# Kernel optimization log

Hardware: AMD Instinct MI355X
Metric: run time of the kernel (lower is better)

## Reference

```python
import jax, jax.numpy as jnp
import numpy as np
from functools import partial

V, CTX, D, H, L, FF = 50257, 1024, 768, 12, 12, 3072
DH = D // H
EPS = 1e-5


def _ln(x, g, b):
    m = jnp.mean(x, axis=-1, keepdims=True)
    v = jnp.mean(jnp.square(x - m), axis=-1, keepdims=True)
    return (x - m) * jax.lax.rsqrt(v + EPS) * g + b


def setup_inputs() -> dict:
    key = jax.random.key(0)
    ks = jax.random.split(key, 8)
    s = 0.02
    return {
        "input_ids": jax.random.randint(ks[0], (2, 1024), 0, V),
        "token_emb": jax.random.normal(ks[1], (V, D), jnp.float32) * s,
        "pos_emb": jax.random.normal(ks[2], (CTX, D), jnp.float32) * s,
        "ln1_g": jnp.ones((L, D), jnp.float32),
        "ln1_b": jnp.zeros((L, D), jnp.float32),
        "qkv_w": jax.random.normal(ks[3], (L, 3 * D, D), jnp.float32) * s,
        "out_w": jax.random.normal(ks[4], (L, D, D), jnp.float32) * (s / np.sqrt(2 * L)),
        "ln2_g": jnp.ones((L, D), jnp.float32),
        "ln2_b": jnp.zeros((L, D), jnp.float32),
        "ff1_w": jax.random.normal(ks[5], (L, FF, D), jnp.float32) * s,
        "ff2_w": jax.random.normal(ks[6], (L, D, FF), jnp.float32) * s,
        "lnf_g": jnp.ones((D,), jnp.float32),
        "lnf_b": jnp.zeros((D,), jnp.float32),
    }


def reference(input_ids, token_emb, pos_emb, ln1_g, ln1_b, qkv_w, out_w,
              ln2_g, ln2_b, ff1_w, ff2_w, lnf_g, lnf_b):
    B, T = input_ids.shape
    x = token_emb[input_ids] + pos_emb[:T]  # [B,T,D]
    causal = jnp.tril(jnp.ones((T, T), bool))  # True = keep
    scale = 1.0 / np.sqrt(DH)

    def block(x, p):
        g1, b1, wqkv, wo, g2, b2, w1, w2 = p
        h = _ln(x, g1, b1)
        qkv = h @ wqkv.T  # [B,T,3D]
        q, k, v = jnp.split(qkv, 3, axis=-1)
        q = q.reshape(B, T, H, DH).transpose(0, 2, 1, 3)
        k = k.reshape(B, T, H, DH).transpose(0, 2, 1, 3)
        v = v.reshape(B, T, H, DH).transpose(0, 2, 1, 3)
        scores = jnp.einsum('bhqd,bhkd->bhqk', q, k) * scale
        scores = jnp.where(causal, scores, -jnp.inf)
        w = jax.nn.softmax(scores, axis=-1)
        o = jnp.einsum('bhqk,bhkd->bhqd', w, v)
        o = o.transpose(0, 2, 1, 3).reshape(B, T, D) @ wo.T
        x = x + o
        h2 = _ln(x, g2, b2)
        ff = jax.nn.gelu(h2 @ w1.T, approximate=False) @ w2.T
        return x + ff, None

    params = (ln1_g, ln1_b, qkv_w, out_w, ln2_g, ln2_b, ff1_w, ff2_w)
    x, _ = jax.lax.scan(block, x, params)
    x = _ln(x, lnf_g, lnf_b)
    logits = x @ token_emb.T  # tied lm head
    return logits
```

## Files before the change

kernel.cpp:

```cpp
#include <hip/hip_runtime.h>
#include <hip/hip_bf16.h>
#include <math.h>

#define D_MODEL 768
#define NHEAD 12
#define DHEAD 64
#define NLAYER 12
#define FF_DIM 3072
#define SEQ 1024
#define TOKENS 2048
#define VOCAB 50257

typedef short bf16x8 __attribute__((ext_vector_type(8)));
typedef float f32x4 __attribute__((ext_vector_type(4)));
typedef unsigned short u16x4 __attribute__((ext_vector_type(4)));
typedef unsigned short u16x8 __attribute__((ext_vector_type(8)));

__device__ inline unsigned short f2bf(float f) {
    union { float f; unsigned u; } un;
    un.f = f;
    unsigned u = un.u;
    u += 0x7fffu + ((u >> 16) & 1u);
    return (unsigned short)(u >> 16);
}

__device__ inline void gl_lds16(const void* g, void* l) {
    __builtin_amdgcn_global_load_lds(
        (const __attribute__((address_space(1))) unsigned int*)g,
        (__attribute__((address_space(3))) unsigned int*)l, 16, 0, 0);
}

__global__ __launch_bounds__(256) void cvt_kernel(const float* __restrict__ s,
                                                  unsigned short* __restrict__ d,
                                                  long n4) {
    long i = (long)blockIdx.x * 256 + threadIdx.x;
    long stride = (long)gridDim.x * 256;
    for (; i < n4; i += stride) {
        f32x4 v = ((const f32x4*)s)[i];
        u16x4 r;
        r[0] = f2bf(v[0]); r[1] = f2bf(v[1]); r[2] = f2bf(v[2]); r[3] = f2bf(v[3]);
        ((u16x4*)d)[i] = r;
    }
}

__global__ __launch_bounds__(256) void embed_kernel(const int* __restrict__ ids,
                                                    const float* __restrict__ tok,
                                                    const float* __restrict__ pos,
                                                    float* __restrict__ x) {
    int i = blockIdx.x * 256 + threadIdx.x;
    int row = i / D_MODEL;
    int d = i - row * D_MODEL;
    int t = row & (SEQ - 1);
    x[i] = tok[(long)ids[row] * D_MODEL + d] + pos[(long)t * D_MODEL + d];
}

__global__ __launch_bounds__(256) void ln_kernel(const float* __restrict__ x,
                                                 const float* __restrict__ g,
                                                 const float* __restrict__ b,
                                                 unsigned short* __restrict__ out) {
    int row = blockIdx.x;
    int tid = threadIdx.x;
    const float* xr = x + (long)row * D_MODEL;
    float v0 = xr[tid], v1 = xr[tid + 256], v2 = xr[tid + 512];
    __shared__ float sm[4];
    float s = v0 + v1 + v2;
    #pragma unroll
    for (int off = 32; off; off >>= 1) s += __shfl_xor(s, off);
    if ((tid & 63) == 0) sm[tid >> 6] = s;
    __syncthreads();
    float mean = (sm[0] + sm[1] + sm[2] + sm[3]) * (1.f / D_MODEL);
    __syncthreads();
    float d0 = v0 - mean, d1 = v1 - mean, d2 = v2 - mean;
    s = d0 * d0 + d1 * d1 + d2 * d2;
    #pragma unroll
    for (int off = 32; off; off >>= 1) s += __shfl_xor(s, off);
    if ((tid & 63) == 0) sm[tid >> 6] = s;
    __syncthreads();
    float var = (sm[0] + sm[1] + sm[2] + sm[3]) * (1.f / D_MODEL);
    float rs = rsqrtf(var + 1e-5f);
    unsigned short* orow = out + (long)row * D_MODEL;
    orow[tid]       = f2bf(d0 * rs * g[tid]       + b[tid]);
    orow[tid + 256] = f2bf(d1 * rs * g[tid + 256] + b[tid + 256]);
    orow[tid + 512] = f2bf(d2 * rs * g[tid + 512] + b[tid + 512]);
}

#define GM_NONE 0
#define GM_RES  1
#define GM_GELU 2
#define GM_QKV  3

template<int WM, int WN, int MODE, bool SWZ>
__global__ __launch_bounds__(256) void gemm_bf16(
        const unsigned short* __restrict__ A, const unsigned short* __restrict__ W,
        int M, int N, int K,
        float* __restrict__ Cf, unsigned short* __restrict__ Cb,
        const float* __restrict__ RES,
        unsigned short* __restrict__ P1, unsigned short* __restrict__ P2) {
    constexpr int BM = WM * 32, BN = WN * 32;
    __shared__ unsigned short lA[BM * 64];
    __shared__ unsigned short lB[BN * 64];

    int tid = threadIdx.x;
    int lane = tid & 63, wv = tid >> 6;
    int wr = wv >> 1, wc = wv & 1;
    int lr = lane & 15, kq = lane >> 4;

    int mtile, ntile;
    if (SWZ) {
        int lb = blockIdx.y * gridDim.x + blockIdx.x;
        int g = lb >> 3, r8 = lb & 7;
        mtile = g % gridDim.x;
        ntile = (g / gridDim.x) * 8 + r8;
        if (ntile * BN >= N) return;
    } else {
        mtile = blockIdx.x;
        ntile = blockIdx.y;
    }
    int row0 = mtile * BM;
    int col0 = ntile * BN;

    int srow_in = tid >> 3;
    int ssp = tid & 7;
    int skg = ssp ^ (srow_in & 7);
    int lbase = ((tid & ~63)) << 3;

    f32x4 acc[WM][WN];
    #pragma unroll
    for (int m = 0; m < WM; m++)
        #pragma unroll
        for (int n = 0; n < WN; n++) acc[m][n] = (f32x4){0.f, 0.f, 0.f, 0.f};

    for (int kt = 0; kt < K; kt += 64) {
        #pragma unroll
        for (int i = 0; i < BM / 32; i++) {
            int row = i * 32 + srow_in;
            gl_lds16(A + (size_t)(row0 + row) * K + kt + skg * 8,
                     &lA[i * 2048 + lbase]);
        }
        #pragma unroll
        for (int i = 0; i < BN / 32; i++) {
            int row = i * 32 + srow_in;
            int srow = col0 + row;
            if (srow >= N) srow = N - 1;
            gl_lds16(W + (size_t)srow * K + kt + skg * 8,
                     &lB[i * 2048 + lbase]);
        }
        __syncthreads();
        #pragma unroll
        for (int kk = 0; kk < 2; kk++) {
            int kg = kk * 4 + kq;
            bf16x8 af[WM], bfr[WN];
            #pragma unroll
            for (int m = 0; m < WM; m++) {
                int row = wr * (WM * 16) + m * 16 + lr;
                af[m] = *(const bf16x8*)&lA[row * 64 + ((kg ^ (row & 7)) << 3)];
            }
            #pragma unroll
            for (int n = 0; n < WN; n++) {
                int row = wc * (WN * 16) + n * 16 + lr;
                bfr[n] = *(const bf16x8*)&lB[row * 64 + ((kg ^ (row & 7)) << 3)];
            }
            #pragma unroll
            for (int m = 0; m < WM; m++)
                #pragma unroll
                for (int n = 0; n < WN; n++)
                    acc[m][n] = __builtin_amdgcn_mfma_f32_16x16x32_bf16(af[m], bfr[n], acc[m][n], 0, 0, 0);
        }
        __syncthreads();
    }

    #pragma unroll
    for (int m = 0; m < WM; m++) {
        int r0 = row0 + wr * (WM * 16) + m * 16 + (kq << 2);
        #pragma unroll
        for (int n = 0; n < WN; n++) {
            int c = col0 + wc * (WN * 16) + n * 16 + lr;
            if (c < N) {
                #pragma unroll
                for (int j = 0; j < 4; j++) {
                    int r = r0 + j;
                    size_t idx = (size_t)r * N + c;
                    float v = acc[m][n][j];
                    if (MODE == GM_RES) {
                        Cf[idx] = v + RES[idx];
                    } else if (MODE == GM_GELU) {
                        Cb[idx] = f2bf(0.5f * v * (1.f + erff(v * 0.70710678118f)));
                    } else if (MODE == GM_QKV) {
                        int bb = r >> 10, t = r & 1023;
                        if (c < D_MODEL) {
                            int h = c >> 6, dh = c & 63;
                            P1[(((size_t)(bb * NHEAD + h) * SEQ) + t) * 64 + dh] = f2bf(v * 0.125f);
                        } else if (c < 2 * D_MODEL) {
                            int cc = c - D_MODEL;
                            int h = cc >> 6, dh = cc & 63;
                            P2[(((size_t)(bb * NHEAD + h) * SEQ) + t) * 64 + dh] = f2bf(v);
                        } else {
                            Cb[(size_t)r * D_MODEL + (c - 2 * D_MODEL)] = f2bf(v);
                        }
                    } else {
                        Cf[idx] = v;
                    }
                }
            }
        }
    }
}

__global__ __launch_bounds__(256) void vprep_kernel(const unsigned short* __restrict__ Vrow,
                                                    unsigned short* __restrict__ Vt) {
    __shared__ unsigned short T[64][66];
    int b = blockIdx.z, h = blockIdx.y, t0 = blockIdx.x * 64;
    int tid = threadIdx.x;
    int tin = tid >> 2, seg = tid & 3;
    const unsigned short* src = Vrow + ((size_t)(b * SEQ) + t0 + tin) * D_MODEL
                                + h * 64 + seg * 16;
    u16x8 a0 = *(const u16x8*)src;
    u16x8 a1 = *(const u16x8*)(src + 8);
    #pragma unroll
    for (int e = 0; e < 8; e++) { T[tin][seg * 16 + e] = a0[e]; T[tin][seg * 16 + 8 + e] = a1[e]; }
    __syncthreads();
    int dh = tid >> 2;
    unsigned short* dst = Vt + ((size_t)(b * NHEAD + h) * 64 + dh) * SEQ + t0 + seg * 16;
    u16x8 o0, o1;
    #pragma unroll
    for (int e = 0; e < 8; e++) o0[e] = T[seg * 16 + e][dh];
    #pragma unroll
    for (int e = 0; e < 8; e++) o1[e] = T[seg * 16 + 8 + e][dh];
    *(u16x8*)dst = o0;
    *(u16x8*)(dst + 8) = o1;
}

#define ANW 4
__global__ __launch_bounds__(256) void attn_mfma(const unsigned short* __restrict__ Qb,
                                                 const unsigned short* __restrict__ Kb,
                                                 const unsigned short* __restrict__ Vt,
                                                 unsigned short* __restrict__ att) {
    int b = blockIdx.z, h = blockIdx.y, pr = blockIdx.x;
    int tid = threadIdx.x, l = tid & 63, w = tid >> 6;
    int lr = l & 15, hg = l >> 4;
    int hk8 = hg * 8, hg4 = hg * 4;
    size_t bh = (size_t)b * NHEAD + h;
    const unsigned short* Qp = Qb + bh * SEQ * 64;
    const unsigned short* Kp = Kb + bh * SEQ * 64;
    const unsigned short* Vp = Vt + bh * 64 * SEQ;

    __shared__ float sm_m[ANW][2][16], sm_l[ANW][2][16];
    __shared__ float sm_o[ANW][2][16][65];
    __shared__ unsigned short pl[ANW][1024];
    unsigned short* Pw = &pl[w][0];

    #pragma unroll
    for (int ti = 0; ti < 2; ti++) {
        int tile = ti ? (63 - pr) : pr;
        int q0 = tile * 16;
        bf16x8 qf0 = *(const bf16x8*)(Qp + (size_t)(q0 + lr) * 64 + hk8);
        bf16x8 qf1 = *(const bf16x8*)(Qp + (size_t)(q0 + lr) * 64 + 32 + hk8);
        f32x4 O[4];
        #pragma unroll
        for (int dt = 0; dt < 4; dt++) O[dt] = (f32x4){0.f, 0.f, 0.f, 0.f};
        f32x4 mrun = (f32x4){-1e30f, -1e30f, -1e30f, -1e30f};
        f32x4 lrun = (f32x4){0.f, 0.f, 0.f, 0.f};
        int nch = (tile >> 2) + 1;

        for (int c = w; c < nch; c += ANW) {
            int k0 = c * 64;
            f32x4 S[4];
            #pragma unroll
            for (int kt = 0; kt < 4; kt++) {
                S[kt] = (f32x4){0.f, 0.f, 0.f, 0.f};
                bf16x8 kf = *(const bf16x8*)(Kp + (size_t)(k0 + kt * 16 + lr) * 64 + hk8);
                S[kt] = __builtin_amdgcn_mfma_f32_16x16x32_bf16(qf0, kf, S[kt], 0, 0, 0);
                kf = *(const bf16x8*)(Kp + (size_t)(k0 + kt * 16 + lr) * 64 + 32 + hk8);
                S[kt] = __builtin_amdgcn_mfma_f32_16x16x32_bf16(qf1, kf, S[kt], 0, 0, 0);
            }
            if (c == nch - 1) {
                #pragma unroll
                for (int kt = 0; kt < 4; kt++)
                    #pragma unroll
                    for (int j = 0; j < 4; j++)
                        S[kt][j] = (k0 + kt * 16 + lr <= q0 + hg4 + j) ? S[kt][j] : -3.0e38f;
            }
            f32x4 rm;
            #pragma unroll
            for (int j = 0; j < 4; j++)
                rm[j] = fmaxf(fmaxf(S[0][j], S[1][j]), fmaxf(S[2][j], S[3][j]));
            #pragma unroll
            for (int msk = 1; msk <= 8; msk <<= 1)
                #pragma unroll
                for (int j = 0; j < 4; j++)
                    rm[j] = fmaxf(rm[j], __shfl_xor(rm[j], msk));
            f32x4 mn, corr, rs;
            #pragma unroll
            for (int j = 0; j < 4; j++) {
                mn[j] = fmaxf(mrun[j], rm[j]);
                corr[j] = __expf(mrun[j] - mn[j]);
                rs[j] = 0.f;
            }
            #pragma unroll
            for (int kt = 0; kt < 4; kt++)
                #pragma unroll
                for (int j = 0; j < 4; j++) {
                    float p = __expf(S[kt][j] - mn[j]);
                    S[kt][j] = p;
                    rs[j] += p;
                }
            #pragma unroll
            for (int msk = 1; msk <= 8; msk <<= 1)
                #pragma unroll
                for (int j = 0; j < 4; j++)
                    rs[j] += __shfl_xor(rs[j], msk);
            #pragma unroll
            for (int j = 0; j < 4; j++) {
                lrun[j] = lrun[j] * corr[j] + rs[j];
                mrun[j] = mn[j];
            }
            #pragma unroll
            for (int dt = 0; dt < 4; dt++)
                #pragma unroll
                for (int j = 0; j < 4; j++) O[dt][j] *= corr[j];
            #pragma unroll
            for (int kt = 0; kt < 4; kt++) {
                int cc = kt * 16 + lr;
                int slot = cc >> 3, off = cc & 7;
                #pragma unroll
                for (int j = 0; j < 4; j++) {
                    int r = hg4 + j;
                    Pw[r * 64 + ((slot ^ (r & 7)) << 3) + off] = f2bf(S[kt][j]);
                }
            }
            asm volatile("s_waitcnt lgkmcnt(0)" ::: "memory");
            bf16x8 pf0 = *(const bf16x8*)&Pw[lr * 64 + ((hg ^ (lr & 7)) << 3)];
            bf16x8 pf1 = *(const bf16x8*)&Pw[lr * 64 + (((4 + hg) ^ (lr & 7)) << 3)];
            #pragma unroll
            for (int dt = 0; dt < 4; dt++) {
                bf16x8 vf = *(const bf16x8*)(Vp + (size_t)(dt * 16 + lr) * SEQ + k0 + hk8);
                O[dt] = __builtin_amdgcn_mfma_f32_16x16x32_bf16(pf0, vf, O[dt], 0, 0, 0);
                vf = *(const bf16x8*)(Vp + (size_t)(dt * 16 + lr) * SEQ + k0 + 32 + hk8);
                O[dt] = __builtin_amdgcn_mfma_f32_16x16x32_bf16(pf1, vf, O[dt], 0, 0, 0);
            }
        }
        if (lr == 0) {
            #pragma unroll
            for (int j = 0; j < 4; j++) {
                sm_m[w][ti][hg4 + j] = mrun[j];
                sm_l[w][ti][hg4 + j] = lrun[j];
            }
        }
        #pragma unroll
        for (int dt = 0; dt < 4; dt++)
            #pragma unroll
            for (int j = 0; j < 4; j++)
                sm_o[w][ti][hg4 + j][dt * 16 + lr] = O[dt][j];
    }
    __syncthreads();
    {
        int ti2 = w >> 1;
        int tile = ti2 ? (63 - pr) : pr;
        int q0 = tile * 16;
        #pragma unroll
        for (int jj = 0; jj < 2; jj++) {
            int j = (w & 1) * 2 + jj;
            int r = hg4 + j;
            float m0 = sm_m[0][ti2][r], m1 = sm_m[1][ti2][r];
            float m2 = sm_m[2][ti2][r], m3 = sm_m[3][ti2][r];
            float M = fmaxf(fmaxf(m0, m1), fmaxf(m2, m3));
            float e0 = __expf(m0 - M), e1 = __expf(m1 - M);
            float e2 = __expf(m2 - M), e3 = __expf(m3 - M);
            float L = sm_l[0][ti2][r] * e0 + sm_l[1][ti2][r] * e1
                    + sm_l[2][ti2][r] * e2 + sm_l[3][ti2][r] * e3;
            float invL = 1.f / L;
            unsigned short* orow = att + ((size_t)(b * SEQ + q0 + r)) * D_MODEL + h * 64;
            #pragma unroll
            for (int dt = 0; dt < 4; dt++) {
                int cidx = dt * 16 + lr;
                float o = sm_o[0][ti2][r][cidx] * e0 + sm_o[1][ti2][r][cidx] * e1
                        + sm_o[2][ti2][r][cidx] * e2 + sm_o[3][ti2][r][cidx] * e3;
                orow[cidx] = f2bf(o * invL);
            }
        }
    }
}

extern "C" void kernel_launch(void* const* d_in, const int* in_sizes, int n_in,
                              void* d_out, int out_size, void* d_ws, size_t ws_size,
                              hipStream_t stream) {
    const int*   input_ids = (const int*)d_in[0];
    const float* token_emb = (const float*)d_in[1];
    const float* pos_emb   = (const float*)d_in[2];
    const float* ln1_g     = (const float*)d_in[3];
    const float* ln1_b     = (const float*)d_in[4];
    const float* qkv_w     = (const float*)d_in[5];
    const float* out_w     = (const float*)d_in[6];
    const float* ln2_g     = (const float*)d_in[7];
    const float* ln2_b     = (const float*)d_in[8];
    const float* ff1_w     = (const float*)d_in[9];
    const float* ff2_w     = (const float*)d_in[10];
    const float* lnf_g     = (const float*)d_in[11];
    const float* lnf_b     = (const float*)d_in[12];
    float* out = (float*)d_out;

    const size_t SZ_QKV_L = (size_t)3 * D_MODEL * D_MODEL;
    const size_t SZ_OUT_L = (size_t)D_MODEL * D_MODEL;
    const size_t SZ_FF1_L = (size_t)FF_DIM * D_MODEL;
    const size_t SZ_FF2_L = (size_t)D_MODEL * FF_DIM;
    const size_t SZ_TOK   = (size_t)VOCAB * D_MODEL;

    char* base = (char*)d_ws;
    size_t off = 0;
    auto alloc = [&](size_t bytes) -> char* {
        char* p = base + off;
        off = (off + bytes + 255) & ~(size_t)255;
        return p;
    };

    float* x              = (float*)alloc((size_t)TOKENS * D_MODEL * 4);
    unsigned short* hb    = (unsigned short*)alloc((size_t)TOKENS * D_MODEL * 2);
    unsigned short* attb  = (unsigned short*)alloc((size_t)TOKENS * D_MODEL * 2);
    unsigned short* ffab  = (unsigned short*)alloc((size_t)TOKENS * FF_DIM * 2);
    unsigned short* Qb    = (unsigned short*)alloc((size_t)TOKENS * D_MODEL * 2);
    unsigned short* Kb    = (unsigned short*)alloc((size_t)TOKENS * D_MODEL * 2);
    unsigned short* Vrow  = (unsigned short*)alloc((size_t)TOKENS * D_MODEL * 2);
    unsigned short* Vtb   = (unsigned short*)alloc((size_t)TOKENS * D_MODEL * 2);

    size_t act_end = off;
    size_t full_need = act_end + 2 * (NLAYER * (SZ_QKV_L + SZ_OUT_L + SZ_FF1_L + SZ_FF2_L) + SZ_TOK)
                       + 6 * 256;
    bool full = ws_size >= full_need;

    unsigned short *qkvA, *outA, *ff1A, *ff2A, *tokA;
    if (full) {
        qkvA = (unsigned short*)alloc(2 * NLAYER * SZ_QKV_L);
        outA = (unsigned short*)alloc(2 * NLAYER * SZ_OUT_L);
        ff1A = (unsigned short*)alloc(2 * NLAYER * SZ_FF1_L);
        ff2A = (unsigned short*)alloc(2 * NLAYER * SZ_FF2_L);
        tokA = (unsigned short*)alloc(2 * SZ_TOK);
    } else {
        qkvA = (unsigned short*)alloc(2 * SZ_QKV_L);
        outA = (unsigned short*)alloc(2 * SZ_OUT_L);
        ff1A = (unsigned short*)alloc(2 * SZ_FF1_L);
        ff2A = (unsigned short*)alloc(2 * SZ_FF2_L);
        tokA = (unsigned short*)alloc(2 * SZ_TOK);
    }

    auto cvt = [&](const float* s, unsigned short* d, size_t n) {
        long n4 = (long)(n / 4);
        int g = (int)((n4 + 255) / 256);
        if (g > 2048) g = 2048;
        cvt_kernel<<<g, 256, 0, stream>>>(s, d, n4);
    };

    if (full) {
        cvt(qkv_w, qkvA, NLAYER * SZ_QKV_L);
        cvt(out_w, outA, NLAYER * SZ_OUT_L);
        cvt(ff1_w, ff1A, NLAYER * SZ_FF1_L);
        cvt(ff2_w, ff2A, NLAYER * SZ_FF2_L);
        cvt(token_emb, tokA, SZ_TOK);
    }

    embed_kernel<<<TOKENS * D_MODEL / 256, 256, 0, stream>>>(input_ids, token_emb, pos_emb, x);

    for (int l = 0; l < NLAYER; l++) {
        const unsigned short* qw = full ? qkvA + (size_t)l * SZ_QKV_L : qkvA;
        const unsigned short* ow = full ? outA + (size_t)l * SZ_OUT_L : outA;
        const unsigned short* f1 = full ? ff1A + (size_t)l * SZ_FF1_L : ff1A;
        const unsigned short* f2 = full ? ff2A + (size_t)l * SZ_FF2_L : ff2A;

        ln_kernel<<<TOKENS, 256, 0, stream>>>(x, ln1_g + l * D_MODEL, ln1_b + l * D_MODEL, hb);
        if (!full) cvt(qkv_w + (size_t)l * SZ_QKV_L, qkvA, SZ_QKV_L);
        gemm_bf16<2, 4, GM_QKV, false><<<dim3(TOKENS / 64, 3 * D_MODEL / 128), 256, 0, stream>>>(
            hb, qw, TOKENS, 3 * D_MODEL, D_MODEL, nullptr, Vrow, nullptr, Qb, Kb);
        vprep_kernel<<<dim3(SEQ / 64, NHEAD, 2), 256, 0, stream>>>(Vrow, Vtb);
        attn_mfma<<<dim3(32, NHEAD, 2), 256, 0, stream>>>(Qb, Kb, Vtb, attb);
        if (!full) cvt(out_w + (size_t)l * SZ_OUT_L, outA, SZ_OUT_L);
        gemm_bf16<2, 4, GM_RES, false><<<dim3(TOKENS / 64, D_MODEL / 128), 256, 0, stream>>>(
            attb, ow, TOKENS, D_MODEL, D_MODEL, x, nullptr, x, nullptr, nullptr);
        ln_kernel<<<TOKENS, 256, 0, stream>>>(x, ln2_g + l * D_MODEL, ln2_b + l * D_MODEL, hb);
        if (!full) cvt(ff1_w + (size_t)l * SZ_FF1_L, ff1A, SZ_FF1_L);
        gemm_bf16<2, 4, GM_GELU, false><<<dim3(TOKENS / 64, FF_DIM / 128), 256, 0, stream>>>(
            hb, f1, TOKENS, FF_DIM, D_MODEL, nullptr, ffab, nullptr, nullptr, nullptr);
        if (!full) cvt(ff2_w + (size_t)l * SZ_FF2_L, ff2A, SZ_FF2_L);
        gemm_bf16<2, 4, GM_RES, false><<<dim3(TOKENS / 64, D_MODEL / 128), 256, 0, stream>>>(
            ffab, f2, TOKENS, D_MODEL, FF_DIM, x, nullptr, x, nullptr, nullptr);
    }

    ln_kernel<<<TOKENS, 256, 0, stream>>>(x, lnf_g, lnf_b, hb);
    if (!full) cvt(token_emb, tokA, SZ_TOK);
    gemm_bf16<4, 4, GM_NONE, true><<<dim3(TOKENS / 128, 400), 256, 0, stream>>>(
        hb, tokA, TOKENS, VOCAB, D_MODEL, out, nullptr, nullptr, nullptr, nullptr);
}
```

Before: 2.417 ms.

## Double-buffer LM-head GEMM LDS tiles, drop swizzle, shrink residual GEMM tiles

Adds a template option that double-buffers the LDS A/B tiles so the next K-tile's global-to-LDS loads are issued while the current tile is being multiplied. The LM-head GEMM uses this mode, and its grouped block swizzle is replaced by a plain grid. The two residual GEMMs (out-proj and FF2) move to smaller 64x64 tiles, which doubles their block count for better CU occupancy. The cost is twice the LDS for the LM-head kernel, which may lower occupancy, plus the loss of L2 locality that the swizzle provided.

Result: faster. 2.211 ms (-8.5%).

```diff
diff --git a/kernel.cpp b/kernel.cpp
--- a/kernel.cpp
+++ b/kernel.cpp
@@ -89,7 +89,7 @@
 #define GM_GELU 2
 #define GM_QKV  3
 
-template<int WM, int WN, int MODE, bool SWZ>
+template<int WM, int WN, int MODE, int DB>
 __global__ __launch_bounds__(256) void gemm_bf16(
         const unsigned short* __restrict__ A, const unsigned short* __restrict__ W,
         int M, int N, int K,
@@ -97,27 +97,15 @@
         const float* __restrict__ RES,
         unsigned short* __restrict__ P1, unsigned short* __restrict__ P2) {
     constexpr int BM = WM * 32, BN = WN * 32;
-    __shared__ unsigned short lA[BM * 64];
-    __shared__ unsigned short lB[BN * 64];
+    __shared__ unsigned short lA[DB][BM * 64];
+    __shared__ unsigned short lB[DB][BN * 64];
 
     int tid = threadIdx.x;
     int lane = tid & 63, wv = tid >> 6;
     int wr = wv >> 1, wc = wv & 1;
     int lr = lane & 15, kq = lane >> 4;
-
-    int mtile, ntile;
-    if (SWZ) {
-        int lb = blockIdx.y * gridDim.x + blockIdx.x;
-        int g = lb >> 3, r8 = lb & 7;
-        mtile = g % gridDim.x;
-        ntile = (g / gridDim.x) * 8 + r8;
-        if (ntile * BN >= N) return;
-    } else {
-        mtile = blockIdx.x;
-        ntile = blockIdx.y;
-    }
-    int row0 = mtile * BM;
-    int col0 = ntile * BN;
+    int row0 = blockIdx.x * BM;
+    int col0 = blockIdx.y * BN;
 
     int srow_in = tid >> 3;
     int ssp = tid & 7;
@@ -130,12 +118,12 @@
         #pragma unroll
         for (int n = 0; n < WN; n++) acc[m][n] = (f32x4){0.f, 0.f, 0.f, 0.f};
 
-    for (int kt = 0; kt < K; kt += 64) {
+    auto stage = [&](int buf, int kt) {
         #pragma unroll
         for (int i = 0; i < BM / 32; i++) {
             int row = i * 32 + srow_in;
             gl_lds16(A + (size_t)(row0 + row) * K + kt + skg * 8,
-                     &lA[i * 2048 + lbase]);
+                     &lA[buf][i * 2048 + lbase]);
         }
         #pragma unroll
         for (int i = 0; i < BN / 32; i++) {
@@ -143,9 +131,10 @@
             int srow = col0 + row;
             if (srow >= N) srow = N - 1;
             gl_lds16(W + (size_t)srow * K + kt + skg * 8,
-                     &lB[i * 2048 + lbase]);
-        }
-        __syncthreads();
+                     &lB[buf][i * 2048 + lbase]);
+        }
+    };
+    auto compute = [&](int buf) {
         #pragma unroll
         for (int kk = 0; kk < 2; kk++) {
             int kg = kk * 4 + kq;
@@ -153,12 +142,12 @@
             #pragma unroll
             for (int m = 0; m < WM; m++) {
                 int row = wr * (WM * 16) + m * 16 + lr;
-                af[m] = *(const bf16x8*)&lA[row * 64 + ((kg ^ (row & 7)) << 3)];
+                af[m] = *(const bf16x8*)&lA[buf][row * 64 + ((kg ^ (row & 7)) << 3)];
             }
             #pragma unroll
             for (int n = 0; n < WN; n++) {
                 int row = wc * (WN * 16) + n * 16 + lr;
-                bfr[n] = *(const bf16x8*)&lB[row * 64 + ((kg ^ (row & 7)) << 3)];
+                bfr[n] = *(const bf16x8*)&lB[buf][row * 64 + ((kg ^ (row & 7)) << 3)];
             }
             #pragma unroll
             for (int m = 0; m < WM; m++)
@@ -166,7 +155,26 @@
                 for (int n = 0; n < WN; n++)
                     acc[m][n] = __builtin_amdgcn_mfma_f32_16x16x32_bf16(af[m], bfr[n], acc[m][n], 0, 0, 0);
         }
+    };
+
+    if (DB == 2) {
+        stage(0, 0);
         __syncthreads();
+        int nt = K >> 6;
+        int cur = 0;
+        for (int t = 0; t < nt; t++) {
+            if (t + 1 < nt) stage(cur ^ 1, (t + 1) << 6);
+            compute(cur);
+            __syncthreads();
+            cur ^= 1;
+        }
+    } else {
+        for (int kt = 0; kt < K; kt += 64) {
+            stage(0, kt);
+            __syncthreads();
+            compute(0);
+            __syncthreads();
+        }
     }
 
     #pragma unroll
@@ -467,24 +475,24 @@
 
         ln_kernel<<<TOKENS, 256, 0, stream>>>(x, ln1_g + l * D_MODEL, ln1_b + l * D_MODEL, hb);
         if (!full) cvt(qkv_w + (size_t)l * SZ_QKV_L, qkvA, SZ_QKV_L);
-        gemm_bf16<2, 4, GM_QKV, false><<<dim3(TOKENS / 64, 3 * D_MODEL / 128), 256, 0, stream>>>(
+        gemm_bf16<2, 4, GM_QKV, 1><<<dim3(TOKENS / 64, 3 * D_MODEL / 128), 256, 0, stream>>>(
             hb, qw, TOKENS, 3 * D_MODEL, D_MODEL, nullptr, Vrow, nullptr, Qb, Kb);
         vprep_kernel<<<dim3(SEQ / 64, NHEAD, 2), 256, 0, stream>>>(Vrow, Vtb);
         attn_mfma<<<dim3(32, NHEAD, 2), 256, 0, stream>>>(Qb, Kb, Vtb, attb);
         if (!full) cvt(out_w + (size_t)l * SZ_OUT_L, outA, SZ_OUT_L);
-        gemm_bf16<2, 4, GM_RES, false><<<dim3(TOKENS / 64, D_MODEL / 128), 256, 0, stream>>>(
+        gemm_bf16<2, 2, GM_RES, 1><<<dim3(TOKENS / 64, D_MODEL / 64), 256, 0, stream>>>(
             attb, ow, TOKENS, D_MODEL, D_MODEL, x, nullptr, x, nullptr, nullptr);
         ln_kernel<<<TOKENS, 256, 0, stream>>>(x, ln2_g + l * D_MODEL, ln2_b + l * D_MODEL, hb);
         if (!full) cvt(ff1_w + (size_t)l * SZ_FF1_L, ff1A, SZ_FF1_L);
-        gemm_bf16<2, 4, GM_GELU, false><<<dim3(TOKENS / 64, FF_DIM / 128), 256, 0, stream>>>(
+        gemm_bf16<2, 4, GM_GELU, 1><<<dim3(TOKENS / 64, FF_DIM / 128), 256, 0, stream>>>(
             hb, f1, TOKENS, FF_DIM, D_MODEL, nullptr, ffab, nullptr, nullptr, nullptr);
         if (!full) cvt(ff2_w + (size_t)l * SZ_FF2_L, ff2A, SZ_FF2_L);
-        gemm_bf16<2, 4, GM_RES, false><<<dim3(TOKENS / 64, D_MODEL / 128), 256, 0, stream>>>(
+        gemm_bf16<2, 2, GM_RES, 1><<<dim3(TOKENS / 64, D_MODEL / 64), 256, 0, stream>>>(
             ffab, f2, TOKENS, D_MODEL, FF_DIM, x, nullptr, x, nullptr, nullptr);
     }
 
     ln_kernel<<<TOKENS, 256, 0, stream>>>(x, lnf_g, lnf_b, hb);
     if (!full) cvt(token_emb, tokA, SZ_TOK);
-    gemm_bf16<4, 4, GM_NONE, true><<<dim3(TOKENS / 128, 400), 256, 0, stream>>>(
+    gemm_bf16<4, 4, GM_NONE, 2><<<dim3(TOKENS / 128, (VOCAB + 127) / 128), 256, 0, stream>>>(
         hb, tokA, TOKENS, VOCAB, D_MODEL, out, nullptr, nullptr, nullptr, nullptr);
 }
```
